# Optimization experiments

Hardware: AMD Instinct MI355X
Metric: run time of the kernel (lower is better)

Reference implementation:

```python
import jax, jax.numpy as jnp
import numpy as np
import math

NEG = -9.0e15
LN_EPS = 1e-5


def _segment_masks(x_ids, pad_idx, sep_idx):
    # x_ids: [B, L] int
    B, L = x_ids.shape
    valid = x_ids != pad_idx                       # [B, L]
    sep_mask = x_ids == sep_idx
    has_sep = jnp.any(sep_mask, axis=1)            # [B]
    first_sep = jnp.argmax(sep_mask, axis=1)       # argmax of bool == first True
    valid_len = valid.sum(axis=1)
    fallback = jnp.clip(valid_len // 2, 1, max(1, L - 2))
    sep_pos = jnp.where(has_sep, first_sep, fallback)  # [B]
    pos = jnp.arange(L)[None, :]                   # [1, L]
    false_mask = (pos < sep_pos[:, None]) & valid  # tokens before SEP
    option_mask = (pos > sep_pos[:, None]) & valid # tokens after SEP
    return false_mask, option_mask


def _masked_softmax(logits, mask):
    return jax.nn.softmax(jnp.where(mask, logits, NEG), axis=-1)


def _forward(x, x_ids, pad_idx, sep_idx,
             w_anom, b_anom,
             w_sq, b_sq, w_sk, b_sk,
             w_cq, b_cq, w_ck, b_ck,
             w_rq, b_rq, w_rk, b_rk,
             w_f1, b_f1, w_f2, b_f2, ln_g, ln_b):
    B, L, D = x.shape
    false_mask, option_mask = _segment_masks(x_ids, pad_idx, sep_idx)

    # anomaly gate over false-sentence tokens
    anomaly_logits = (x @ w_anom + b_anom)[..., 0]                 # [B, L]
    gate = jax.nn.softmax(jnp.where(false_mask, anomaly_logits, NEG), axis=1)
    gate = gate * false_mask.astype(x.dtype)
    gate = gate / jnp.clip(gate.sum(axis=1, keepdims=True), 1e-8)  # [B, L]

    scale = 1.0 / math.sqrt(D)
    q_sup = x @ w_sq + b_sq
    k_sup = x @ w_sk + b_sk
    q_con = x @ w_cq + b_cq
    k_con = x @ w_ck + b_ck
    q_rep = x @ w_rq + b_rq
    k_rep = x @ w_rk + b_rk

    support_scores = jnp.einsum('bid,bjd->bij', q_sup, k_sup) * scale  # [B, L, L]
    conflict_scores = jnp.einsum('bid,bjd->bij', q_con, k_con) * scale
    repair_scores = jnp.einsum('bid,bjd->bij', q_rep, k_rep) * scale

    pair_mask = false_mask[:, :, None] & option_mask[:, None, :]       # [B, L, L]
    support_attn = _masked_softmax(support_scores, pair_mask)
    repair_attn = _masked_softmax(repair_scores + jnp.tanh(conflict_scores), pair_mask)

    repair_token_vec = jnp.einsum('bij,bjd->bid', repair_attn, x)      # [B, L, D]
    support_token_vec = jnp.einsum('bij,bjd->bid', support_attn, x)

    anomaly_false_vec = jnp.einsum('bl,bld->bd', gate, x)
    weighted_repair_vec = jnp.einsum('bl,bld->bd', gate, repair_token_vec)
    weighted_support_vec = jnp.einsum('bl,bld->bd', gate, support_token_vec)

    fused = jnp.concatenate([anomaly_false_vec, weighted_repair_vec, weighted_support_vec], axis=-1)
    fused = jax.nn.relu(fused @ w_f1 + b_f1) @ w_f2 + b_f2            # [B, D] (dropout=eval no-op)

    mu = fused.mean(axis=-1, keepdims=True)
    var = fused.var(axis=-1, keepdims=True)
    fused = (fused - mu) / jnp.sqrt(var + LN_EPS) * ln_g + ln_b
    return fused


def setup_inputs() -> dict:
    key = jax.random.key(0)
    B, L, D = 32, 512, 1024
    ks = jax.random.split(key, 16)
    s = 0.02
    inp = {
        'x': jax.random.normal(ks[0], (B, L, D), dtype=jnp.float32),
        'x_ids': jax.random.randint(ks[1], (B, L), 0, 30000, dtype=jnp.int32),
        'pad_idx': 0,
        'sep_idx': 102,
        'w_anom': jax.random.normal(ks[2], (D, 1), dtype=jnp.float32) * s,
        'b_anom': jnp.zeros((1,), jnp.float32),
        'w_sq': jax.random.normal(ks[3], (D, D), dtype=jnp.float32) * s,
        'b_sq': jnp.zeros((D,), jnp.float32),
        'w_sk': jax.random.normal(ks[4], (D, D), dtype=jnp.float32) * s,
        'b_sk': jnp.zeros((D,), jnp.float32),
        'w_cq': jax.random.normal(ks[5], (D, D), dtype=jnp.float32) * s,
        'b_cq': jnp.zeros((D,), jnp.float32),
        'w_ck': jax.random.normal(ks[6], (D, D), dtype=jnp.float32) * s,
        'b_ck': jnp.zeros((D,), jnp.float32),
        'w_rq': jax.random.normal(ks[7], (D, D), dtype=jnp.float32) * s,
        'b_rq': jnp.zeros((D,), jnp.float32),
        'w_rk': jax.random.normal(ks[8], (D, D), dtype=jnp.float32) * s,
        'b_rk': jnp.zeros((D,), jnp.float32),
        'w_f1': jax.random.normal(ks[9], (3 * D, D), dtype=jnp.float32) * s,
        'b_f1': jnp.zeros((D,), jnp.float32),
        'w_f2': jax.random.normal(ks[10], (D, D), dtype=jnp.float32) * s,
        'b_f2': jnp.zeros((D,), jnp.float32),
        'ln_g': jnp.ones((D,), jnp.float32),
        'ln_b': jnp.zeros((D,), jnp.float32),
    }
    return inp


def reference(x, x_ids, pad_idx, sep_idx,
              w_anom, b_anom, w_sq, b_sq, w_sk, b_sk, w_cq, b_cq, w_ck, b_ck,
              w_rq, b_rq, w_rk, b_rk, w_f1, b_f1, w_f2, b_f2, ln_g, ln_b):
    return _forward(x, x_ids, pad_idx, sep_idx,
                    w_anom, b_anom, w_sq, b_sq, w_sk, b_sk, w_cq, b_cq,
                    w_ck, b_ck, w_rq, b_rq, w_rk, b_rk,
                    w_f1, b_f1, w_f2, b_f2, ln_g, ln_b)
```

## Files before the change

kernel.cpp:

```cpp
#include <hip/hip_runtime.h>
#include <cmath>
#include <cstdint>

static constexpr int kB = 32;
static constexpr int kL = 512;
static constexpr int kD = 1024;
static constexpr int kNT = kB * kL;
#define NEGF (-9.0e15f)
#define SCALE 0.03125f

typedef __bf16 bf16x8 __attribute__((ext_vector_type(8)));
typedef __bf16 bf16x4 __attribute__((ext_vector_type(4)));
typedef float f32x4 __attribute__((ext_vector_type(4)));

__device__ __forceinline__ float wave_sum(float v){
#pragma unroll
  for(int o=32;o>0;o>>=1) v += __shfl_xor(v,o,64);
  return v;
}
__device__ __forceinline__ float wave_max(float v){
#pragma unroll
  for(int o=32;o>0;o>>=1) v = fmaxf(v,__shfl_xor(v,o,64));
  return v;
}
template<int NW>
__device__ __forceinline__ float blk_sum(float v, float* red){
  v = wave_sum(v);
  __syncthreads();
  if((threadIdx.x&63)==0) red[threadIdx.x>>6]=v;
  __syncthreads();
  float r = red[0];
#pragma unroll
  for(int i=1;i<NW;i++) r += red[i];
  return r;
}
template<int NW>
__device__ __forceinline__ float blk_max(float v, float* red){
  v = wave_max(v);
  __syncthreads();
  if((threadIdx.x&63)==0) red[threadIdx.x>>6]=v;
  __syncthreads();
  float r = red[0];
#pragma unroll
  for(int i=1;i<NW;i++) r = fmaxf(r, red[i]);
  return r;
}

__device__ __forceinline__ void gload16(const void* g, void* l){
  __builtin_amdgcn_global_load_lds(
      (const __attribute__((address_space(1))) void*)g,
      (__attribute__((address_space(3))) void*)l, 16, 0, 0);
}

__device__ __forceinline__ void xcd_remap(int gx, int gy, int gz, int& ox, int& oy, int& oz){
  int flat = blockIdx.x + gx*(blockIdx.y + gy*blockIdx.z);
  int nwg = gx*gy*gz;
  int c = flat & 7, j = flat >> 3;
  int logical = c*(nwg >> 3) + j;
  ox = logical % gx; int rest = logical / gx;
  oy = rest % gy; oz = rest / gy;
}

__global__ __launch_bounds__(256) void masks_kernel(
    const int* __restrict__ ids, const int* __restrict__ pad_p, const int* __restrict__ sep_p,
    int* __restrict__ n_fm, int* __restrict__ n_om,
    int* __restrict__ nfs, int* __restrict__ nos,
    unsigned char* __restrict__ fm, unsigned char* __restrict__ om,
    float* __restrict__ c_sup, float* __restrict__ c_rep)
{
  int b = blockIdx.x, t = threadIdx.x;
  int pad = pad_p[0], sep = sep_p[0];
  __shared__ int s_first, s_vl, s_nf, s_no, s_sp;
  __shared__ int s_nfs[4], s_nos[4];
  if (t == 0){ s_first = kL; s_vl = 0; s_nf = 0; s_no = 0; }
  if (t < 4){ s_nfs[t] = 0; s_nos[t] = 0; }
  __syncthreads();
  int id0 = ids[b*kL + t], id1 = ids[b*kL + t + 256];
  int v0 = (id0 != pad) ? 1 : 0, v1 = (id1 != pad) ? 1 : 0;
  int fl = kL;
  if (id0 == sep) fl = t;
  if (id1 == sep && (t + 256) < fl) fl = t + 256;
  atomicMin(&s_first, fl);
  atomicAdd(&s_vl, v0 + v1);
  __syncthreads();
  if (t == 0){
    int vl = s_vl;
    int fb = vl / 2; if (fb < 1) fb = 1; if (fb > kL - 2) fb = kL - 2;
    s_sp = (s_first < kL) ? s_first : fb;
  }
  __syncthreads();
  int sp = s_sp;
  int f0 = ((t < sp) && v0) ? 1 : 0,         o0 = ((t > sp) && v0) ? 1 : 0;
  int f1 = (((t+256) < sp) && v1) ? 1 : 0,   o1 = (((t+256) > sp) && v1) ? 1 : 0;
  fm[b*kL+t] = (unsigned char)f0; fm[b*kL+t+256] = (unsigned char)f1;
  om[b*kL+t] = (unsigned char)o0; om[b*kL+t+256] = (unsigned char)o1;
  atomicAdd(&s_nf, f0 + f1); atomicAdd(&s_no, o0 + o1);
  if (f0) atomicAdd(&s_nfs[t>>7], 1);
  if (o0) atomicAdd(&s_nos[t>>7], 1);
  if (f1) atomicAdd(&s_nfs[(t+256)>>7], 1);
  if (o1) atomicAdd(&s_nos[(t+256)>>7], 1);
  __syncthreads();
  if (t == 0){ n_fm[b] = s_nf; n_om[b] = s_no; }
  if (t < 4){ nfs[b*4 + t] = s_nfs[t]; nos[b*4 + t] = s_nos[t]; }
  float u = (s_no == 0 && s_nf > 0) ? (1.0f/(float)kL) : 0.0f;
  c_sup[b*kL+t] = u; c_sup[b*kL+t+256] = u;
  c_rep[b*kL+t] = u; c_rep[b*kL+t+256] = u;
}

__global__ __launch_bounds__(256) void conv_w_kernel(
    const float* w0, const float* w1, const float* w2,
    const float* w3, const float* w4, const float* w5, __bf16* __restrict__ Wb)
{
  const float* W;
  switch (blockIdx.y){
    case 0: W = w0; break; case 1: W = w1; break; case 2: W = w2; break;
    case 3: W = w3; break; case 4: W = w4; break; default: W = w5; break;
  }
  size_t i = ((size_t)blockIdx.x * 256 + threadIdx.x) * 8;
  float4 a = *reinterpret_cast<const float4*>(W + i);
  float4 b = *reinterpret_cast<const float4*>(W + i + 4);
  bf16x8 v;
  v[0]=(__bf16)a.x; v[1]=(__bf16)a.y; v[2]=(__bf16)a.z; v[3]=(__bf16)a.w;
  v[4]=(__bf16)b.x; v[5]=(__bf16)b.y; v[6]=(__bf16)b.z; v[7]=(__bf16)b.w;
  *reinterpret_cast<bf16x8*>(Wb + (size_t)blockIdx.y * kD * kD + i) = v;
}

__global__ __launch_bounds__(256) void wb_vec_kernel(
    const float* wsk, const float* bsq, const float* wrk, const float* brq,
    const float* wck, const float* bcq, const float* wcq, const float* bck,
    float* __restrict__ vecs4)
{
  int m = blockIdx.y; const float* M; const float* v;
  switch(m){
    case 0: M=wsk; v=bsq; break; case 1: M=wrk; v=brq; break;
    case 2: M=wck; v=bcq; break; default: M=wcq; v=bck; break;
  }
  int e = blockIdx.x*4 + (threadIdx.x>>6);
  int lane = threadIdx.x & 63;
  const float4* Mr = reinterpret_cast<const float4*>(M + (size_t)e*kD);
  const float4* vr = reinterpret_cast<const float4*>(v);
  float acc = 0.f;
#pragma unroll 4
  for (int i = lane; i < kD/4; i += 64){
    float4 a = Mr[i], w = vr[i];
    acc += a.x*w.x + a.y*w.y + a.z*w.z + a.w*w.w;
  }
  acc = wave_sum(acc);
  if (lane == 0) vecs4[m*kD + e] = acc;
}

__global__ __launch_bounds__(64) void scon_kernel(const float* __restrict__ bcq,
    const float* __restrict__ bck, float* __restrict__ scon_s)
{
  int lane = threadIdx.x;
  float acc = 0.f;
  for (int i = lane; i < kD; i += 64) acc += bcq[i]*bck[i];
  acc = wave_sum(acc);
  if (lane == 0) scon_s[0] = acc;
}

__global__ __launch_bounds__(256) void prep_x_kernel(
    const float* __restrict__ x, const float* __restrict__ w_anom, const float* __restrict__ b_anom,
    const float* __restrict__ vecs4, __bf16* __restrict__ xb,
    float* __restrict__ logits, float* __restrict__ tokc)
{
  int w = threadIdx.x >> 6;
  int row = blockIdx.x*2 + (threadIdx.x>>7);
  int li = threadIdx.x & 127;
  size_t base = (size_t)row*kD + li*8;
  float4 a = *reinterpret_cast<const float4*>(x + base);
  float4 b4 = *reinterpret_cast<const float4*>(x + base + 4);
  bf16x8 v;
  v[0]=(__bf16)a.x; v[1]=(__bf16)a.y; v[2]=(__bf16)a.z; v[3]=(__bf16)a.w;
  v[4]=(__bf16)b4.x; v[5]=(__bf16)b4.y; v[6]=(__bf16)b4.z; v[7]=(__bf16)b4.w;
  *reinterpret_cast<bf16x8*>(xb + base) = v;

  const float* vp[5] = {w_anom, vecs4, vecs4+kD, vecs4+2*kD, vecs4+3*kD};
  float d[5];
#pragma unroll
  for (int j = 0; j < 5; j++){
    float4 wa = *reinterpret_cast<const float4*>(vp[j] + li*8);
    float4 wb2 = *reinterpret_cast<const float4*>(vp[j] + li*8 + 4);
    d[j] = a.x*wa.x + a.y*wa.y + a.z*wa.z + a.w*wa.w
         + b4.x*wb2.x + b4.y*wb2.y + b4.z*wb2.z + b4.w*wb2.w;
    d[j] = wave_sum(d[j]);
  }
  __shared__ float red[4][5];
  if ((threadIdx.x & 63) == 0){
#pragma unroll
    for (int j = 0; j < 5; j++) red[w][j] = d[j];
  }
  __syncthreads();
  if ((threadIdx.x & 127) == 0){
    int w0 = (threadIdx.x >> 7) * 2;
    logits[row] = red[w0][0] + red[w0+1][0] + b_anom[0];
#pragma unroll
    for (int j = 1; j < 5; j++)
      tokc[(j-1)*kNT + row] = red[w0][j] + red[w0+1][j];
  }
}

__global__ __launch_bounds__(256) void gate_kernel(const float* __restrict__ logits,
    const unsigned char* __restrict__ fm, const int* __restrict__ n_fm, float* __restrict__ gate)
{
  int b = blockIdx.x, t = threadIdx.x;
  __shared__ float red[4];
  if (n_fm[b] == 0){ gate[b*kL+t] = 0.f; gate[b*kL+t+256] = 0.f; return; }
  int f0 = fm[b*kL+t], f1 = fm[b*kL+t+256];
  float l0 = f0 ? logits[b*kL+t]     : -INFINITY;
  float l1 = f1 ? logits[b*kL+t+256] : -INFINITY;
  float m = blk_max<4>(fmaxf(l0, l1), red);
  float e0 = f0 ? expf(l0 - m) : 0.f;
  float e1 = f1 ? expf(l1 - m) : 0.f;
  float Z = blk_sum<4>(e0 + e1, red);
  gate[b*kL+t]     = e0 / Z;
  gate[b*kL+t+256] = e1 / Z;
}

__device__ __forceinline__ void gemm_core_p3(
    const __bf16* __restrict__ A, const __bf16* __restrict__ B,
    int m0, int n0, f32x4 (&acc)[4][4], __bf16* smem)
{
  const int tid = threadIdx.x, lane = tid & 63, wid = tid >> 6;
  const int wm = (wid >> 1) * 64, wn = (wid & 1) * 64;
  const int r2 = tid >> 2, sphys = tid & 3;
  const int c2 = ((sphys ^ ((r2 >> 1) & 3)) * 8);
  const __bf16* a0 = A + (size_t)(m0 + r2) * kD + c2;
  const __bf16* a1 = A + (size_t)(m0 + 64 + r2) * kD + c2;
  const __bf16* b0 = B + (size_t)(n0 + r2) * kD + c2;
  const __bf16* b1 = B + (size_t)(n0 + 64 + r2) * kD + c2;
  const int dst0 = r2*32 + sphys*8;
  const int dst1 = (64 + r2)*32 + sphys*8;
  const int lr = lane & 15;
  const int tslot = (((lane >> 4) ^ ((lr >> 1) & 3)) * 8);

  auto stage = [&](__bf16* buf, int k0){
    gload16(a0 + k0, buf + dst0);
    gload16(a1 + k0, buf + dst1);
    gload16(b0 + k0, buf + 4096 + dst0);
    gload16(b1 + k0, buf + 4096 + dst1);
  };
  auto compute = [&](const __bf16* buf){
    const __bf16* As = buf;
    const __bf16* Bs = buf + 4096;
    bf16x8 af[4], bfr[4];
#pragma unroll
    for (int m = 0; m < 4; m++) af[m]  = *reinterpret_cast<const bf16x8*>(As + (wm + m*16 + lr)*32 + tslot);
#pragma unroll
    for (int n = 0; n < 4; n++) bfr[n] = *reinterpret_cast<const bf16x8*>(Bs + (wn + n*16 + lr)*32 + tslot);
#pragma unroll
    for (int n = 0; n < 4; n++)
#pragma unroll
      for (int m = 0; m < 4; m++)
        acc[n][m] = __builtin_amdgcn_mfma_f32_16x16x32_bf16(bfr[n], af[m], acc[n][m], 0, 0, 0);
  };

  __bf16* bc = smem;
  __bf16* bn = smem + 8192;
  __bf16* bs = smem + 16384;

  constexpr int NT = kD / 32;
  stage(bc, 0);
  stage(bn, 32);
  for (int t = 0; t < NT - 2; ++t){
    stage(bs, (t + 2) * 32);
    asm volatile("s_waitcnt vmcnt(8)" ::: "memory");
    __builtin_amdgcn_s_barrier();
    compute(bc);
    __builtin_amdgcn_s_barrier();
    __bf16* tmp = bc; bc = bn; bn = bs; bs = tmp;
  }
  asm volatile("s_waitcnt vmcnt(4)" ::: "memory");
  __builtin_amdgcn_s_barrier();
  compute(bc);
  asm volatile("s_waitcnt vmcnt(0)" ::: "memory");
  __builtin_amdgcn_s_barrier();
  compute(bn);
}


__global__ __launch_bounds__(256) void combine_gemm(
    const __bf16* __restrict__ Wb, __bf16* __restrict__ Bmat)
{
  int bx, by, bz; xcd_remap(8, 8, 3, bx, by, bz);
  int s = bz;
  const __bf16* A = Wb + (size_t)(2*s+1) * kD * kD;
  const __bf16* B = Wb + (size_t)(2*s)   * kD * kD;
  __bf16* O = Bmat + (size_t)s * kD * kD;
  int m0 = by * 128, n0 = bx * 128;
  __shared__ __bf16 smem[3*8192];
  f32x4 acc[4][4] = {};
  gemm_core_p3(A, B, m0, n0, acc, smem);
  const int lane = threadIdx.x & 63, wid = threadIdx.x >> 6;
  const int wm = (wid >> 1) * 64, wn = (wid & 1) * 64;
  const int row_l = wm + (lane & 15), col_l = wn + ((lane >> 4) << 2);
#pragma unroll
  for (int n = 0; n < 4; n++)
#pragma unroll
    for (int m = 0; m < 4; m++){
      int row = m0 + row_l + m*16;
      int colb = n0 + col_l + n*16;
      bf16x4 o;
#pragma unroll
      for (int r = 0; r < 4; r++) o[r] = (__bf16)acc[n][m][r];
      *reinterpret_cast<bf16x4*>(O + (size_t)row * kD + colb) = o;
    }
}

__global__ __launch_bounds__(256) void proj_gemm(
    const __bf16* __restrict__ xb, const __bf16* __restrict__ Bmat,
    const int* __restrict__ nfs, __bf16* __restrict__ P, int b0, int cs)
{
  int bx, by, bz; xcd_remap(8, gridDim.y, 3, bx, by, bz);
  int z = bz;
  int m0 = by * 128, n0 = bx * 128;
  int bi = m0 >> 9, stripe = (m0 >> 7) & 3;
  if (nfs[(b0 + bi)*4 + stripe] == 0) return;
  const __bf16* A = xb + (size_t)b0 * kL * kD;
  const __bf16* B = Bmat + (size_t)z * kD * kD;
  __shared__ __bf16 smem[3*8192];
  f32x4 acc[4][4] = {};
  gemm_core_p3(A, B, m0, n0, acc, smem);
  __bf16* O = P + (size_t)z * cs * kL * kD;
  const int lane = threadIdx.x & 63, wid = threadIdx.x >> 6;
  const int wm = (wid >> 1) * 64, wn = (wid & 1) * 64;
  const int row_l = wm + (lane & 15), col_l = wn + ((lane >> 4) << 2);
#pragma unroll
  for (int n = 0; n < 4; n++)
#pragma unroll
    for (int m = 0; m < 4; m++){
      int row = m0 + row_l + m*16;
      int colb = n0 + col_l + n*16;
      bf16x4 o;
#pragma unroll
      for (int r = 0; r < 4; r++) o[r] = (__bf16)acc[n][m][r];
      *reinterpret_cast<bf16x4*>(O + (size_t)row * kD + colb) = o;
    }
}

__global__ __launch_bounds__(256) void score_gemm(
    const __bf16* __restrict__ P, const __bf16* __restrict__ xb,
    const int* __restrict__ nfs, const int* __restrict__ nos,
    float* __restrict__ S, int b0, int cs)
{
  int bx, by, bz; xcd_remap(4, 4, gridDim.z, bx, by, bz);
  int s = bz % 3, bi = bz / 3;
  int b = b0 + bi;
  if (nfs[b*4 + by] == 0 || nos[b*4 + bx] == 0) return;
  int m0 = by * 128, n0 = bx * 128;
  const __bf16* A = P + ((size_t)s * cs + bi) * kL * kD;
  const __bf16* B = xb + (size_t)b * kL * kD;
  float* O = S + ((size_t)s * cs + bi) * kL * kL;
  __shared__ __bf16 smem[3*8192];
  f32x4 acc[4][4] = {};
  gemm_core_p3(A, B, m0, n0, acc, smem);
  const int lane = threadIdx.x & 63, wid = threadIdx.x >> 6;
  const int wm = (wid >> 1) * 64, wn = (wid & 1) * 64;
  const int row_l = wm + (lane & 15), col_l = wn + ((lane >> 4) << 2);
#pragma unroll
  for (int n = 0; n < 4; n++)
#pragma unroll
    for (int m = 0; m < 4; m++){
      int row = m0 + row_l + m*16;
      int colb = n0 + col_l + n*16;
      f32x4 v = acc[n][m] * SCALE;
      *reinterpret_cast<f32x4*>(O + (size_t)row * kL + colb) = v;
    }
}

__global__ __launch_bounds__(256) void softmax_combine(
    const float* __restrict__ S, const float* __restrict__ gate,
    const unsigned char* __restrict__ om, const int* __restrict__ n_om,
    const float* __restrict__ tokc, const float* __restrict__ scon_s,
    float* __restrict__ c_sup, float* __restrict__ c_rep, int b0, int cs)
{
  int bi = blockIdx.y, b = b0 + bi;
  if (n_om[b] == 0) return;
  int t = threadIdx.x, w = t >> 6, lane = t & 63;
  int c0 = lane * 8;
  const float* ssup = S + ((size_t)0 * cs + bi) * (size_t)kL * kL;
  const float* scon = S + ((size_t)1 * cs + bi) * (size_t)kL * kL;
  const float* srep = S + ((size_t)2 * cs + bi) * (size_t)kL * kL;
  unsigned long long omv = *reinterpret_cast<const unsigned long long*>(om + (size_t)b*kL + c0);
  float csup_c[8], crep_c[8], ccon_c[8];
  bool msk[8];
#pragma unroll
  for (int u = 0; u < 8; u++){
    msk[u] = ((omv >> (8*u)) & 1ull) != 0;
    csup_c[u] = SCALE * tokc[0*kNT + b*kL + c0 + u];
    crep_c[u] = SCALE * tokc[1*kNT + b*kL + c0 + u];
    ccon_c[u] = SCALE * tokc[2*kNT + b*kL + c0 + u];
  }
  float sconst = SCALE * scon_s[0];
  float accS[8] = {}, accR[8] = {};
  int i_base = blockIdx.x * 32 + w * 8;
  for (int ii = 0; ii < 8; ii++){
    int i = i_base + ii;
    float g = gate[(size_t)b*kL + i];
    if (!(g > 0.f)) continue;
    float rcon_i = SCALE * tokc[3*kNT + b*kL + i] + sconst;
    size_t base = (size_t)i * kL + c0;
    f32x4 s0 = *reinterpret_cast<const f32x4*>(ssup + base);
    f32x4 s1 = *reinterpret_cast<const f32x4*>(ssup + base + 4);
    f32x4 cn0 = *reinterpret_cast<const f32x4*>(scon + base);
    f32x4 cn1 = *reinterpret_cast<const f32x4*>(scon + base + 4);
    f32x4 r0 = *reinterpret_cast<const f32x4*>(srep + base);
    f32x4 r1 = *reinterpret_cast<const f32x4*>(srep + base + 4);
    float vs[8], vr[8];
#pragma unroll
    for (int u = 0; u < 8; u++){
      float sv = (u < 4) ? s0[u] : s1[u-4];
      float cv = (u < 4) ? cn0[u] : cn1[u-4];
      float rv = (u < 4) ? r0[u] : r1[u-4];
      vs[u] = msk[u] ? (sv + csup_c[u]) : NEGF;
      vr[u] = msk[u] ? (rv + crep_c[u] + tanhf(cv + ccon_c[u] + rcon_i)) : NEGF;
    }
    float ms = vs[0], mr = vr[0];
#pragma unroll
    for (int u = 1; u < 8; u++){ ms = fmaxf(ms, vs[u]); mr = fmaxf(mr, vr[u]); }
    ms = wave_max(ms); mr = wave_max(mr);
    float es[8], er[8], zs = 0.f, zr = 0.f;
#pragma unroll
    for (int u = 0; u < 8; u++){
      es[u] = expf(vs[u] - ms); er[u] = expf(vr[u] - mr);
      zs += es[u]; zr += er[u];
    }
    zs = wave_sum(zs); zr = wave_sum(zr);
    float gs = g / zs, gr = g / zr;
#pragma unroll
    for (int u = 0; u < 8; u++){ accS[u] += gs * es[u]; accR[u] += gr * er[u]; }
  }
  __shared__ float lsS[4][kL];
  __shared__ float lsR[4][kL];
#pragma unroll
  for (int u = 0; u < 8; u++){ lsS[w][c0+u] = accS[u]; lsR[w][c0+u] = accR[u]; }
  __syncthreads();
  int col0 = t, col1 = t + 256;
  float vS0 = lsS[0][col0]+lsS[1][col0]+lsS[2][col0]+lsS[3][col0];
  float vR0 = lsR[0][col0]+lsR[1][col0]+lsR[2][col0]+lsR[3][col0];
  float vS1 = lsS[0][col1]+lsS[1][col1]+lsS[2][col1]+lsS[3][col1];
  float vR1 = lsR[0][col1]+lsR[1][col1]+lsR[2][col1]+lsR[3][col1];
  atomicAdd(&c_sup[(size_t)b*kL + col0], vS0);
  atomicAdd(&c_rep[(size_t)b*kL + col0], vR0);
  atomicAdd(&c_sup[(size_t)b*kL + col1], vS1);
  atomicAdd(&c_rep[(size_t)b*kL + col1], vR1);
}

__global__ __launch_bounds__(256) void vec_kernel(
    const float* __restrict__ x, const float* __restrict__ gate,
    const float* __restrict__ c_sup, const float* __restrict__ c_rep,
    float* __restrict__ insG)
{
  int b = blockIdx.y;
  int d = blockIdx.x * 256 + threadIdx.x;
  int l0 = blockIdx.z * 128;
  __shared__ float g_s[128], cs_s[128], cr_s[128];
  if (threadIdx.x < 128){
    int l = l0 + threadIdx.x;
    g_s[threadIdx.x]  = gate[b*kL + l];
    cs_s[threadIdx.x] = c_sup[b*kL + l];
    cr_s[threadIdx.x] = c_rep[b*kL + l];
  }
  __syncthreads();
  float a = 0.f, r = 0.f, s = 0.f;
  const float* xb = x + (size_t)b * kL * kD + (size_t)l0 * kD + d;
#pragma unroll 4
  for (int l = 0; l < 128; l++){
    float xv = xb[(size_t)l * kD];
    a = fmaf(g_s[l],  xv, a);
    r = fmaf(cr_s[l], xv, r);
    s = fmaf(cs_s[l], xv, s);
  }
  atomicAdd(&insG[(size_t)(0*kD + d)*kB + b], a);
  atomicAdd(&insG[(size_t)(1*kD + d)*kB + b], r);
  atomicAdd(&insG[(size_t)(2*kD + d)*kB + b], s);
}

__global__ __launch_bounds__(256) void ffn1_kernel(
    const float* __restrict__ insG, const float* __restrict__ w_f1, float* __restrict__ hacc)
{
  int o = blockIdx.x * 64 + (threadIdx.x & 63);
  int bg = threadIdx.x >> 6;
  int k0 = blockIdx.y * 256;
  float acc[8] = {};
  const float* ip = insG + (size_t)k0 * kB + bg * 8;
  const float* wp = w_f1 + (size_t)k0 * kD + o;
#pragma unroll 4
  for (int k = 0; k < 256; k++){
    f32x4 i0 = *reinterpret_cast<const f32x4*>(ip + (size_t)k * kB);
    f32x4 i1 = *reinterpret_cast<const f32x4*>(ip + (size_t)k * kB + 4);
    float wv = wp[(size_t)k * kD];
#pragma unroll
    for (int j = 0; j < 4; j++){ acc[j] = fmaf(i0[j], wv, acc[j]); acc[4+j] = fmaf(i1[j], wv, acc[4+j]); }
  }
#pragma unroll
  for (int j = 0; j < 8; j++) atomicAdd(&hacc[(size_t)(bg*8 + j)*kD + o], acc[j]);
}

__global__ __launch_bounds__(256) void hT_kernel(
    const float* __restrict__ hacc, const float* __restrict__ b_f1, float* __restrict__ hT)
{
  int idx = blockIdx.x * 256 + threadIdx.x;
  int b = idx >> 10, k = idx & 1023;
  float v = hacc[(size_t)b*kD + k] + b_f1[k];
  hT[(size_t)k*kB + b] = fmaxf(v, 0.f);
}

__global__ __launch_bounds__(256) void ffn2_kernel(
    const float* __restrict__ hT, const float* __restrict__ w_f2, float* __restrict__ f2acc)
{
  int o = blockIdx.x * 64 + (threadIdx.x & 63);
  int bg = threadIdx.x >> 6;
  int k0 = blockIdx.y * 256;
  float acc[8] = {};
  const float* ip = hT + (size_t)k0 * kB + bg * 8;
  const float* wp = w_f2 + (size_t)k0 * kD + o;
#pragma unroll 4
  for (int k = 0; k < 256; k++){
    f32x4 i0 = *reinterpret_cast<const f32x4*>(ip + (size_t)k * kB);
    f32x4 i1 = *reinterpret_cast<const f32x4*>(ip + (size_t)k * kB + 4);
    float wv = wp[(size_t)k * kD];
#pragma unroll
    for (int j = 0; j < 4; j++){ acc[j] = fmaf(i0[j], wv, acc[j]); acc[4+j] = fmaf(i1[j], wv, acc[4+j]); }
  }
#pragma unroll
  for (int j = 0; j < 8; j++) atomicAdd(&f2acc[(size_t)(bg*8 + j)*kD + o], acc[j]);
}

__global__ __launch_bounds__(256) void ln_kernel(
    const float* __restrict__ f2acc, const float* __restrict__ b_f2,
    const float* __restrict__ g, const float* __restrict__ bta, float* __restrict__ out)
{
  int b = blockIdx.x, t = threadIdx.x;
  __shared__ float red[4];
  float v[4]; float s1 = 0.f, s2 = 0.f;
#pragma unroll
  for (int u = 0; u < 4; u++){
    int o = t + u*256;
    v[u] = f2acc[(size_t)b*kD + o] + b_f2[o];
    s1 += v[u]; s2 += v[u]*v[u];
  }
  s1 = blk_sum<4>(s1, red);
  s2 = blk_sum<4>(s2, red);
  float mu = s1 * (1.f/(float)kD);
  float var = s2 * (1.f/(float)kD) - mu*mu;
  float inv = rsqrtf(var + 1e-5f);
#pragma unroll
  for (int u = 0; u < 4; u++){
    int o = t + u*256;
    out[(size_t)b*kD + o] = (v[u] - mu) * inv * g[o] + bta[o];
  }
}

extern "C" void kernel_launch(void* const* d_in, const int* in_sizes, int n_in,
                              void* d_out, int out_size, void* d_ws, size_t ws_size,
                              hipStream_t stream)
{
  const float* x      = (const float*)d_in[0];
  const int*   ids    = (const int*)d_in[1];
  const int*   pad_p  = (const int*)d_in[2];
  const int*   sep_p  = (const int*)d_in[3];
  const float* w_anom = (const float*)d_in[4];
  const float* b_anom = (const float*)d_in[5];
  const float* w_sq = (const float*)d_in[6];  const float* b_sq = (const float*)d_in[7];
  const float* w_sk = (const float*)d_in[8];  const float* b_sk = (const float*)d_in[9];
  const float* w_cq = (const float*)d_in[10]; const float* b_cq = (const float*)d_in[11];
  const float* w_ck = (const float*)d_in[12]; const float* b_ck = (const float*)d_in[13];
  const float* w_rq = (const float*)d_in[14]; const float* b_rq = (const float*)d_in[15];
  const float* w_rk = (const float*)d_in[16]; const float* b_rk = (const float*)d_in[17];
  const float* w_f1 = (const float*)d_in[18]; const float* b_f1 = (const float*)d_in[19];
  const float* w_f2 = (const float*)d_in[20]; const float* b_f2 = (const float*)d_in[21];
  const float* lng  = (const float*)d_in[22]; const float* lnb  = (const float*)d_in[23];
  float* out = (float*)d_out;

  char* p = (char*)d_ws;
  auto carve = [&](size_t bytes) -> void* {
    void* r = (void*)p; p += (bytes + 255) & ~(size_t)255; return r;
  };
  int* n_fm = (int*)carve(kB*4);
  int* n_om = (int*)carve(kB*4);
  int* nfs  = (int*)carve(kB*4*4);
  int* nos  = (int*)carve(kB*4*4);
  unsigned char* fm = (unsigned char*)carve(kB*kL);
  unsigned char* om = (unsigned char*)carve(kB*kL);
  float* logits = (float*)carve((size_t)kNT*4);
  float* gate   = (float*)carve((size_t)kNT*4);
  float* c_sup  = (float*)carve((size_t)kNT*4);
  float* c_rep  = (float*)carve((size_t)kNT*4);
  float* tokc   = (float*)carve((size_t)4*kNT*4);
  float* vecs4  = (float*)carve((size_t)4*kD*4);
  float* scon_s = (float*)carve(256);
  float* insG   = (float*)carve((size_t)3*kD*kB*4);
  float* accbuf = (float*)carve((size_t)2*kB*kD*4);
  float* hacc = accbuf, *f2acc = accbuf + (size_t)kB*kD;
  float* hT     = (float*)carve((size_t)kD*kB*4);
  __bf16* Wb   = (__bf16*)carve((size_t)6*kD*kD*2);
  __bf16* Bmat = (__bf16*)carve((size_t)3*kD*kD*2);
  __bf16* xb   = (__bf16*)carve((size_t)kNT*kD*2);

  size_t used = (size_t)(p - (char*)d_ws);
  size_t per_chunk = (size_t)3*kL*kD*2 + (size_t)3*kL*kL*4;
  long avail = (long)ws_size - (long)used - 8192;
  int chunkB = (avail > 0) ? (int)(avail / (long)per_chunk) : 1;
  if (chunkB < 1) chunkB = 1;
  if (chunkB > kB) chunkB = kB;
  __bf16* P      = (__bf16*)carve((size_t)3*chunkB*kL*kD*2);
  float*  scores = (float*) carve((size_t)3*chunkB*kL*kL*4);

  masks_kernel<<<kB, 256, 0, stream>>>(ids, pad_p, sep_p, n_fm, n_om, nfs, nos, fm, om, c_sup, c_rep);
  conv_w_kernel<<<dim3(kD*kD/2048, 6), 256, 0, stream>>>(w_sq, w_sk, w_cq, w_ck, w_rq, w_rk, Wb);
  wb_vec_kernel<<<dim3(kD/4, 4), 256, 0, stream>>>(w_sk, b_sq, w_rk, b_rq, w_ck, b_cq, w_cq, b_ck, vecs4);
  scon_kernel<<<1, 64, 0, stream>>>(b_cq, b_ck, scon_s);
  prep_x_kernel<<<kNT/2, 256, 0, stream>>>(x, w_anom, b_anom, vecs4, xb, logits, tokc);
  gate_kernel<<<kB, 256, 0, stream>>>(logits, fm, n_fm, gate);
  combine_gemm<<<dim3(8, 8, 3), 256, 0, stream>>>(Wb, Bmat);
  hipMemsetAsync(insG, 0, (size_t)(3*kD*kB + 2*kB*kD)*4, stream);

  for (int b0 = 0; b0 < kB; b0 += chunkB){
    int cs = chunkB; if (b0 + cs > kB) cs = kB - b0;
    proj_gemm<<<dim3(8, cs*4, 3), 256, 0, stream>>>(xb, Bmat, nfs, P, b0, cs);
    score_gemm<<<dim3(4, 4, cs*3), 256, 0, stream>>>(P, xb, nfs, nos, scores, b0, cs);
    softmax_combine<<<dim3(kL/32, cs), 256, 0, stream>>>(scores, gate, om, n_om,
        tokc, scon_s, c_sup, c_rep, b0, cs);
  }

  vec_kernel<<<dim3(kD/256, kB, 4), 256, 0, stream>>>(x, gate, c_sup, c_rep, insG);
  ffn1_kernel<<<dim3(kD/64, 12), 256, 0, stream>>>(insG, w_f1, hacc);
  hT_kernel<<<kB*kD/256, 256, 0, stream>>>(hacc, b_f1, hT);
  ffn2_kernel<<<dim3(kD/64, 4), 256, 0, stream>>>(hT, w_f2, f2acc);
  ln_kernel<<<kB, 256, 0, stream>>>(f2acc, b_f2, lng, lnb, out);
}
```

Measured before the change: 293.0 us.

## Store scores as bf16, fuse hT into ffn2, alias Wb with P, read bf16 x

Attention score matrices are now written and read as bf16 instead of fp32, halving their traffic and allowing larger batch chunks. The Wb scratch is aliased with the projection buffer when workspace allows, vec_kernel reads the bf16 copy of x two elements at a time, and the bias+ReLU transpose kernel is folded into ffn2 by having ffn1 write transposed output. tanh and exp use fast approximations. The change lowers precision of the scores and of the x used in the weighted sums.

```diff
diff --git a/kernel.cpp b/kernel.cpp
--- a/kernel.cpp
+++ b/kernel.cpp
@@ -11,6 +11,7 @@
 
 typedef __bf16 bf16x8 __attribute__((ext_vector_type(8)));
 typedef __bf16 bf16x4 __attribute__((ext_vector_type(4)));
+typedef __bf16 bf16x2 __attribute__((ext_vector_type(2)));
 typedef float f32x4 __attribute__((ext_vector_type(4)));
 
 __device__ __forceinline__ float wave_sum(float v){
@@ -50,6 +51,10 @@
   __builtin_amdgcn_global_load_lds(
       (const __attribute__((address_space(1))) void*)g,
       (__attribute__((address_space(3))) void*)l, 16, 0, 0);
+}
+
+__device__ __forceinline__ float fast_tanh(float x){
+  return 1.f - 2.f / (__expf(2.f * x) + 1.f);
 }
 
 __device__ __forceinline__ void xcd_remap(int gx, int gy, int gz, int& ox, int& oy, int& oz){
@@ -210,8 +215,8 @@
   float l0 = f0 ? logits[b*kL+t]     : -INFINITY;
   float l1 = f1 ? logits[b*kL+t+256] : -INFINITY;
   float m = blk_max<4>(fmaxf(l0, l1), red);
-  float e0 = f0 ? expf(l0 - m) : 0.f;
-  float e1 = f1 ? expf(l1 - m) : 0.f;
+  float e0 = f0 ? __expf(l0 - m) : 0.f;
+  float e1 = f1 ? __expf(l1 - m) : 0.f;
   float Z = blk_sum<4>(e0 + e1, red);
   gate[b*kL+t]     = e0 / Z;
   gate[b*kL+t+256] = e1 / Z;
@@ -277,7 +282,6 @@
   __builtin_amdgcn_s_barrier();
   compute(bn);
 }
-
 
 __global__ __launch_bounds__(256) void combine_gemm(
     const __bf16* __restrict__ Wb, __bf16* __restrict__ Bmat)
@@ -341,7 +345,7 @@
 __global__ __launch_bounds__(256) void score_gemm(
     const __bf16* __restrict__ P, const __bf16* __restrict__ xb,
     const int* __restrict__ nfs, const int* __restrict__ nos,
-    float* __restrict__ S, int b0, int cs)
+    __bf16* __restrict__ S, int b0, int cs)
 {
   int bx, by, bz; xcd_remap(4, 4, gridDim.z, bx, by, bz);
   int s = bz % 3, bi = bz / 3;
@@ -350,7 +354,7 @@
   int m0 = by * 128, n0 = bx * 128;
   const __bf16* A = P + ((size_t)s * cs + bi) * kL * kD;
   const __bf16* B = xb + (size_t)b * kL * kD;
-  float* O = S + ((size_t)s * cs + bi) * kL * kL;
+  __bf16* O = S + ((size_t)s * cs + bi) * kL * kL;
   __shared__ __bf16 smem[3*8192];
   f32x4 acc[4][4] = {};
   gemm_core_p3(A, B, m0, n0, acc, smem);
@@ -363,13 +367,15 @@
     for (int m = 0; m < 4; m++){
       int row = m0 + row_l + m*16;
       int colb = n0 + col_l + n*16;
-      f32x4 v = acc[n][m] * SCALE;
-      *reinterpret_cast<f32x4*>(O + (size_t)row * kL + colb) = v;
+      bf16x4 o;
+#pragma unroll
+      for (int r = 0; r < 4; r++) o[r] = (__bf16)(acc[n][m][r] * SCALE);
+      *reinterpret_cast<bf16x4*>(O + (size_t)row * kL + colb) = o;
     }
 }
 
 __global__ __launch_bounds__(256) void softmax_combine(
-    const float* __restrict__ S, const float* __restrict__ gate,
+    const __bf16* __restrict__ S, const float* __restrict__ gate,
     const unsigned char* __restrict__ om, const int* __restrict__ n_om,
     const float* __restrict__ tokc, const float* __restrict__ scon_s,
     float* __restrict__ c_sup, float* __restrict__ c_rep, int b0, int cs)
@@ -378,9 +384,9 @@
   if (n_om[b] == 0) return;
   int t = threadIdx.x, w = t >> 6, lane = t & 63;
   int c0 = lane * 8;
-  const float* ssup = S + ((size_t)0 * cs + bi) * (size_t)kL * kL;
-  const float* scon = S + ((size_t)1 * cs + bi) * (size_t)kL * kL;
-  const float* srep = S + ((size_t)2 * cs + bi) * (size_t)kL * kL;
+  const __bf16* ssup = S + ((size_t)0 * cs + bi) * (size_t)kL * kL;
+  const __bf16* scon = S + ((size_t)1 * cs + bi) * (size_t)kL * kL;
+  const __bf16* srep = S + ((size_t)2 * cs + bi) * (size_t)kL * kL;
   unsigned long long omv = *reinterpret_cast<const unsigned long long*>(om + (size_t)b*kL + c0);
   float csup_c[8], crep_c[8], ccon_c[8];
   bool msk[8];
@@ -400,20 +406,15 @@
     if (!(g > 0.f)) continue;
     float rcon_i = SCALE * tokc[3*kNT + b*kL + i] + sconst;
     size_t base = (size_t)i * kL + c0;
-    f32x4 s0 = *reinterpret_cast<const f32x4*>(ssup + base);
-    f32x4 s1 = *reinterpret_cast<const f32x4*>(ssup + base + 4);
-    f32x4 cn0 = *reinterpret_cast<const f32x4*>(scon + base);
-    f32x4 cn1 = *reinterpret_cast<const f32x4*>(scon + base + 4);
-    f32x4 r0 = *reinterpret_cast<const f32x4*>(srep + base);
-    f32x4 r1 = *reinterpret_cast<const f32x4*>(srep + base + 4);
+    bf16x8 sb = *reinterpret_cast<const bf16x8*>(ssup + base);
+    bf16x8 cb = *reinterpret_cast<const bf16x8*>(scon + base);
+    bf16x8 rb = *reinterpret_cast<const bf16x8*>(srep + base);
     float vs[8], vr[8];
 #pragma unroll
     for (int u = 0; u < 8; u++){
-      float sv = (u < 4) ? s0[u] : s1[u-4];
-      float cv = (u < 4) ? cn0[u] : cn1[u-4];
-      float rv = (u < 4) ? r0[u] : r1[u-4];
+      float sv = (float)sb[u], cv = (float)cb[u], rv = (float)rb[u];
       vs[u] = msk[u] ? (sv + csup_c[u]) : NEGF;
-      vr[u] = msk[u] ? (rv + crep_c[u] + tanhf(cv + ccon_c[u] + rcon_i)) : NEGF;
+      vr[u] = msk[u] ? (rv + crep_c[u] + fast_tanh(cv + ccon_c[u] + rcon_i)) : NEGF;
     }
     float ms = vs[0], mr = vr[0];
 #pragma unroll
@@ -422,7 +423,7 @@
     float es[8], er[8], zs = 0.f, zr = 0.f;
 #pragma unroll
     for (int u = 0; u < 8; u++){
-      es[u] = expf(vs[u] - ms); er[u] = expf(vr[u] - mr);
+      es[u] = __expf(vs[u] - ms); er[u] = __expf(vr[u] - mr);
       zs += es[u]; zr += er[u];
     }
     zs = wave_sum(zs); zr = wave_sum(zr);
@@ -447,12 +448,12 @@
 }
 
 __global__ __launch_bounds__(256) void vec_kernel(
-    const float* __restrict__ x, const float* __restrict__ gate,
+    const __bf16* __restrict__ xb, const float* __restrict__ gate,
     const float* __restrict__ c_sup, const float* __restrict__ c_rep,
     float* __restrict__ insG)
 {
   int b = blockIdx.y;
-  int d = blockIdx.x * 256 + threadIdx.x;
+  int d = (blockIdx.x * 256 + threadIdx.x) * 2;
   int l0 = blockIdx.z * 128;
   __shared__ float g_s[128], cs_s[128], cr_s[128];
   if (threadIdx.x < 128){
@@ -462,22 +463,27 @@
     cr_s[threadIdx.x] = c_rep[b*kL + l];
   }
   __syncthreads();
-  float a = 0.f, r = 0.f, s = 0.f;
-  const float* xb = x + (size_t)b * kL * kD + (size_t)l0 * kD + d;
+  float a0 = 0.f, r0 = 0.f, s0 = 0.f, a1 = 0.f, r1 = 0.f, s1 = 0.f;
+  const __bf16* xp = xb + (size_t)b * kL * kD + (size_t)l0 * kD + d;
 #pragma unroll 4
   for (int l = 0; l < 128; l++){
-    float xv = xb[(size_t)l * kD];
-    a = fmaf(g_s[l],  xv, a);
-    r = fmaf(cr_s[l], xv, r);
-    s = fmaf(cs_s[l], xv, s);
-  }
-  atomicAdd(&insG[(size_t)(0*kD + d)*kB + b], a);
-  atomicAdd(&insG[(size_t)(1*kD + d)*kB + b], r);
-  atomicAdd(&insG[(size_t)(2*kD + d)*kB + b], s);
+    bf16x2 v = *reinterpret_cast<const bf16x2*>(xp + (size_t)l * kD);
+    float x0 = (float)v[0], x1 = (float)v[1];
+    float g = g_s[l], cr = cr_s[l], cspv = cs_s[l];
+    a0 = fmaf(g, x0, a0);   a1 = fmaf(g, x1, a1);
+    r0 = fmaf(cr, x0, r0);  r1 = fmaf(cr, x1, r1);
+    s0 = fmaf(cspv, x0, s0); s1 = fmaf(cspv, x1, s1);
+  }
+  atomicAdd(&insG[(size_t)(0*kD + d)*kB + b], a0);
+  atomicAdd(&insG[(size_t)(1*kD + d)*kB + b], r0);
+  atomicAdd(&insG[(size_t)(2*kD + d)*kB + b], s0);
+  atomicAdd(&insG[(size_t)(0*kD + d + 1)*kB + b], a1);
+  atomicAdd(&insG[(size_t)(1*kD + d + 1)*kB + b], r1);
+  atomicAdd(&insG[(size_t)(2*kD + d + 1)*kB + b], s1);
 }
 
 __global__ __launch_bounds__(256) void ffn1_kernel(
-    const float* __restrict__ insG, const float* __restrict__ w_f1, float* __restrict__ hacc)
+    const float* __restrict__ insG, const float* __restrict__ w_f1, float* __restrict__ hraw)
 {
   int o = blockIdx.x * 64 + (threadIdx.x & 63);
   int bg = threadIdx.x >> 6;
@@ -494,34 +500,32 @@
     for (int j = 0; j < 4; j++){ acc[j] = fmaf(i0[j], wv, acc[j]); acc[4+j] = fmaf(i1[j], wv, acc[4+j]); }
   }
 #pragma unroll
-  for (int j = 0; j < 8; j++) atomicAdd(&hacc[(size_t)(bg*8 + j)*kD + o], acc[j]);
-}
-
-__global__ __launch_bounds__(256) void hT_kernel(
-    const float* __restrict__ hacc, const float* __restrict__ b_f1, float* __restrict__ hT)
-{
-  int idx = blockIdx.x * 256 + threadIdx.x;
-  int b = idx >> 10, k = idx & 1023;
-  float v = hacc[(size_t)b*kD + k] + b_f1[k];
-  hT[(size_t)k*kB + b] = fmaxf(v, 0.f);
+  for (int j = 0; j < 8; j++) atomicAdd(&hraw[(size_t)o*kB + bg*8 + j], acc[j]);
 }
 
 __global__ __launch_bounds__(256) void ffn2_kernel(
-    const float* __restrict__ hT, const float* __restrict__ w_f2, float* __restrict__ f2acc)
+    const float* __restrict__ hraw, const float* __restrict__ b_f1,
+    const float* __restrict__ w_f2, float* __restrict__ f2acc)
 {
   int o = blockIdx.x * 64 + (threadIdx.x & 63);
   int bg = threadIdx.x >> 6;
   int k0 = blockIdx.y * 256;
   float acc[8] = {};
-  const float* ip = hT + (size_t)k0 * kB + bg * 8;
+  const float* ip = hraw + (size_t)k0 * kB + bg * 8;
+  const float* bp = b_f1 + k0;
   const float* wp = w_f2 + (size_t)k0 * kD + o;
 #pragma unroll 4
   for (int k = 0; k < 256; k++){
+    float bv = bp[k];
     f32x4 i0 = *reinterpret_cast<const f32x4*>(ip + (size_t)k * kB);
     f32x4 i1 = *reinterpret_cast<const f32x4*>(ip + (size_t)k * kB + 4);
     float wv = wp[(size_t)k * kD];
 #pragma unroll
-    for (int j = 0; j < 4; j++){ acc[j] = fmaf(i0[j], wv, acc[j]); acc[4+j] = fmaf(i1[j], wv, acc[4+j]); }
+    for (int j = 0; j < 4; j++){
+      float v0 = fmaxf(i0[j] + bv, 0.f);
+      float v1 = fmaxf(i1[j] + bv, 0.f);
+      acc[j] = fmaf(v0, wv, acc[j]); acc[4+j] = fmaf(v1, wv, acc[4+j]);
+    }
   }
 #pragma unroll
   for (int j = 0; j < 8; j++) atomicAdd(&f2acc[(size_t)(bg*8 + j)*kD + o], acc[j]);
@@ -592,41 +596,64 @@
   float* scon_s = (float*)carve(256);
   float* insG   = (float*)carve((size_t)3*kD*kB*4);
   float* accbuf = (float*)carve((size_t)2*kB*kD*4);
-  float* hacc = accbuf, *f2acc = accbuf + (size_t)kB*kD;
-  float* hT     = (float*)carve((size_t)kD*kB*4);
-  __bf16* Wb   = (__bf16*)carve((size_t)6*kD*kD*2);
+  float* hraw = accbuf, *f2acc = accbuf + (size_t)kB*kD;
   __bf16* Bmat = (__bf16*)carve((size_t)3*kD*kD*2);
   __bf16* xb   = (__bf16*)carve((size_t)kNT*kD*2);
 
   size_t used = (size_t)(p - (char*)d_ws);
-  size_t per_chunk = (size_t)3*kL*kD*2 + (size_t)3*kL*kL*4;
+  size_t wb_bytes = (size_t)6*kD*kD*2;
+  size_t per_chunk = (size_t)3*kL*kD*2 + (size_t)3*kL*kL*2;
   long avail = (long)ws_size - (long)used - 8192;
-  int chunkB = (avail > 0) ? (int)(avail / (long)per_chunk) : 1;
-  if (chunkB < 1) chunkB = 1;
-  if (chunkB > kB) chunkB = kB;
-  __bf16* P      = (__bf16*)carve((size_t)3*chunkB*kL*kD*2);
-  float*  scores = (float*) carve((size_t)3*chunkB*kL*kL*4);
-
-  masks_kernel<<<kB, 256, 0, stream>>>(ids, pad_p, sep_p, n_fm, n_om, nfs, nos, fm, om, c_sup, c_rep);
-  conv_w_kernel<<<dim3(kD*kD/2048, 6), 256, 0, stream>>>(w_sq, w_sk, w_cq, w_ck, w_rq, w_rk, Wb);
-  wb_vec_kernel<<<dim3(kD/4, 4), 256, 0, stream>>>(w_sk, b_sq, w_rk, b_rq, w_ck, b_cq, w_cq, b_ck, vecs4);
-  scon_kernel<<<1, 64, 0, stream>>>(b_cq, b_ck, scon_s);
-  prep_x_kernel<<<kNT/2, 256, 0, stream>>>(x, w_anom, b_anom, vecs4, xb, logits, tokc);
-  gate_kernel<<<kB, 256, 0, stream>>>(logits, fm, n_fm, gate);
-  combine_gemm<<<dim3(8, 8, 3), 256, 0, stream>>>(Wb, Bmat);
-  hipMemsetAsync(insG, 0, (size_t)(3*kD*kB + 2*kB*kD)*4, stream);
-
-  for (int b0 = 0; b0 < kB; b0 += chunkB){
-    int cs = chunkB; if (b0 + cs > kB) cs = kB - b0;
-    proj_gemm<<<dim3(8, cs*4, 3), 256, 0, stream>>>(xb, Bmat, nfs, P, b0, cs);
-    score_gemm<<<dim3(4, 4, cs*3), 256, 0, stream>>>(P, xb, nfs, nos, scores, b0, cs);
-    softmax_combine<<<dim3(kL/32, cs), 256, 0, stream>>>(scores, gate, om, n_om,
-        tokc, scon_s, c_sup, c_rep, b0, cs);
-  }
-
-  vec_kernel<<<dim3(kD/256, kB, 4), 256, 0, stream>>>(x, gate, c_sup, c_rep, insG);
-  ffn1_kernel<<<dim3(kD/64, 12), 256, 0, stream>>>(insG, w_f1, hacc);
-  hT_kernel<<<kB*kD/256, 256, 0, stream>>>(hacc, b_f1, hT);
-  ffn2_kernel<<<dim3(kD/64, 4), 256, 0, stream>>>(hT, w_f2, f2acc);
+  __bf16 *Wb, *P, *scores;
+  if (avail >= (long)(wb_bytes) && avail >= (long)per_chunk){
+    int chunkB = (int)(avail / (long)per_chunk);
+    if (chunkB > kB) chunkB = kB;
+    Wb = (__bf16*)p;
+    P  = (__bf16*)p;
+    scores = P + (size_t)3*chunkB*kL*kD;
+    masks_kernel<<<kB, 256, 0, stream>>>(ids, pad_p, sep_p, n_fm, n_om, nfs, nos, fm, om, c_sup, c_rep);
+    conv_w_kernel<<<dim3(kD*kD/2048, 6), 256, 0, stream>>>(w_sq, w_sk, w_cq, w_ck, w_rq, w_rk, Wb);
+    wb_vec_kernel<<<dim3(kD/4, 4), 256, 0, stream>>>(w_sk, b_sq, w_rk, b_rq, w_ck, b_cq, w_cq, b_ck, vecs4);
+    scon_kernel<<<1, 64, 0, stream>>>(b_cq, b_ck, scon_s);
+    prep_x_kernel<<<kNT/2, 256, 0, stream>>>(x, w_anom, b_anom, vecs4, xb, logits, tokc);
+    gate_kernel<<<kB, 256, 0, stream>>>(logits, fm, n_fm, gate);
+    combine_gemm<<<dim3(8, 8, 3), 256, 0, stream>>>(Wb, Bmat);
+    hipMemsetAsync(insG, 0, (size_t)(3*kD*kB + 2*kB*kD)*4, stream);
+    for (int b0 = 0; b0 < kB; b0 += chunkB){
+      int cs = chunkB; if (b0 + cs > kB) cs = kB - b0;
+      proj_gemm<<<dim3(8, cs*4, 3), 256, 0, stream>>>(xb, Bmat, nfs, P, b0, cs);
+      score_gemm<<<dim3(4, 4, cs*3), 256, 0, stream>>>(P, xb, nfs, nos, scores, b0, cs);
+      softmax_combine<<<dim3(kL/32, cs), 256, 0, stream>>>(scores, gate, om, n_om,
+          tokc, scon_s, c_sup, c_rep, b0, cs);
+    }
+  } else {
+    Wb = (__bf16*)carve(wb_bytes);
+    used = (size_t)(p - (char*)d_ws);
+    avail = (long)ws_size - (long)used - 8192;
+    int chunkB = (avail > 0) ? (int)(avail / (long)per_chunk) : 1;
+    if (chunkB < 1) chunkB = 1;
+    if (chunkB > kB) chunkB = kB;
+    P = (__bf16*)p;
+    scores = P + (size_t)3*chunkB*kL*kD;
+    masks_kernel<<<kB, 256, 0, stream>>>(ids, pad_p, sep_p, n_fm, n_om, nfs, nos, fm, om, c_sup, c_rep);
+    conv_w_kernel<<<dim3(kD*kD/2048, 6), 256, 0, stream>>>(w_sq, w_sk, w_cq, w_ck, w_rq, w_rk, Wb);
+    wb_vec_kernel<<<dim3(kD/4, 4), 256, 0, stream>>>(w_sk, b_sq, w_rk, b_rq, w_ck, b_cq, w_cq, b_ck, vecs4);
+    scon_kernel<<<1, 64, 0, stream>>>(b_cq, b_ck, scon_s);
+    prep_x_kernel<<<kNT/2, 256, 0, stream>>>(x, w_anom, b_anom, vecs4, xb, logits, tokc);
+    gate_kernel<<<kB, 256, 0, stream>>>(logits, fm, n_fm, gate);
+    combine_gemm<<<dim3(8, 8, 3), 256, 0, stream>>>(Wb, Bmat);
+    hipMemsetAsync(insG, 0, (size_t)(3*kD*kB + 2*kB*kD)*4, stream);
+    for (int b0 = 0; b0 < kB; b0 += chunkB){
+      int cs = chunkB; if (b0 + cs > kB) cs = kB - b0;
+      proj_gemm<<<dim3(8, cs*4, 3), 256, 0, stream>>>(xb, Bmat, nfs, P, b0, cs);
+      score_gemm<<<dim3(4, 4, cs*3), 256, 0, stream>>>(P, xb, nfs, nos, scores, b0, cs);
+      softmax_combine<<<dim3(kL/32, cs), 256, 0, stream>>>(scores, gate, om, n_om,
+          tokc, scon_s, c_sup, c_rep, b0, cs);
+    }
+  }
+
+  vec_kernel<<<dim3(kD/512, kB, 4), 256, 0, stream>>>(xb, gate, c_sup, c_rep, insG);
+  ffn1_kernel<<<dim3(kD/64, 12), 256, 0, stream>>>(insG, w_f1, hraw);
+  ffn2_kernel<<<dim3(kD/64, 4), 256, 0, stream>>>(hraw, b_f1, w_f2, f2acc);
   ln_kernel<<<kB, 256, 0, stream>>>(f2acc, b_f2, lng, lnb, out);
 }
```

Measured after the change: 307.1 us. 1.05x slower.
